# Performance work log

Measured on AMD Instinct MI355X. Metric: run time of the kernel, lower is better.

## Reference

```python
import jax, jax.numpy as jnp
import numpy as np

B, T, IN_DIM = 32, 512, 16
F_DIM, N_AGG, N_HEADS = 128, 32, 4


def _ln(x, g, b, eps=1e-5):
    m = jnp.mean(x, axis=-1, keepdims=True)
    v = jnp.var(x, axis=-1, keepdims=True)
    return (x - m) * jax.lax.rsqrt(v + eps) * g + b


def _masked_sab(X, mask, wq, bq, wk, bk, wv, bv, wo, bo, g0, be0, g1, be1):
    # Set-Transformer style SAB = MAB(X, X) with key-side masking.
    Bn, Tn, _ = X.shape
    Dh = F_DIM // N_HEADS
    Q = X @ wq + bq
    K = X @ wk + bk
    V = X @ wv + bv
    Qh = Q.reshape(Bn, Tn, N_HEADS, Dh)
    Kh = K.reshape(Bn, Tn, N_HEADS, Dh)
    Vh = V.reshape(Bn, Tn, N_HEADS, Dh)
    scores = jnp.einsum('bqhd,bkhd->bhqk', Qh, Kh) / np.float32(np.sqrt(Dh))
    scores = jnp.where(mask[:, None, None, :] > 0, scores, jnp.float32(-1e9))
    A = jax.nn.softmax(scores, axis=-1)
    O = Q + jnp.einsum('bhqk,bkhd->bqhd', A, Vh).reshape(Bn, Tn, F_DIM)
    O = _ln(O, g0, be0)
    O = O + jax.nn.relu(O @ wo + bo)
    return _ln(O, g1, be1)


def setup_inputs():
    key = jax.random.key(0)
    ks = list(jax.random.split(key, 16))

    def g(k, shape):
        return jax.random.uniform(k, shape, jnp.float32, -1.0, 1.0) / np.float32(np.sqrt(shape[0]))

    inp = {
        'X': jax.random.normal(ks[0], (B, T, IN_DIM), dtype=jnp.float32),
        'mask': jax.random.bernoulli(ks[1], 0.8, (B, T)).astype(jnp.float32),
    }
    i = 2
    for suf, din in (('0', IN_DIM), ('1', F_DIM)):
        kk = jax.random.split(ks[i], 4); i += 1
        inp['wq' + suf] = g(kk[0], (din, F_DIM)); inp['bq' + suf] = jnp.zeros((F_DIM,), jnp.float32)
        inp['wk' + suf] = g(kk[1], (din, F_DIM)); inp['bk' + suf] = jnp.zeros((F_DIM,), jnp.float32)
        inp['wv' + suf] = g(kk[2], (din, F_DIM)); inp['bv' + suf] = jnp.zeros((F_DIM,), jnp.float32)
        inp['wo' + suf] = g(kk[3], (F_DIM, F_DIM)); inp['bo' + suf] = jnp.zeros((F_DIM,), jnp.float32)
        inp['g0' + suf] = jnp.ones((F_DIM,), jnp.float32); inp['be0' + suf] = jnp.zeros((F_DIM,), jnp.float32)
        inp['g1' + suf] = jnp.ones((F_DIM,), jnp.float32); inp['be1' + suf] = jnp.zeros((F_DIM,), jnp.float32)
    inp['wti'] = g(ks[i], (F_DIM, F_DIM)); i += 1
    inp['bti'] = jnp.zeros((F_DIM,), jnp.float32)
    inp['was'] = g(ks[i], (F_DIM, N_AGG)); i += 1
    inp['bas'] = jnp.zeros((N_AGG,), jnp.float32)
    d_cat = 2 * F_DIM * N_AGG + IN_DIM + F_DIM
    inp['wto'] = g(ks[i], (d_cat, F_DIM)); i += 1
    inp['bto'] = jnp.zeros((F_DIM,), jnp.float32)
    inp['gto'] = jnp.ones((F_DIM,), jnp.float32)
    inp['btoln'] = jnp.zeros((F_DIM,), jnp.float32)
    return inp


def reference(X, mask, wq0, bq0, wk0, bk0, wv0, bv0, wo0, bo0, g00, be00, g10, be10,
              wq1, bq1, wk1, bk1, wv1, bv1, wo1, bo1, g01, be01, g11, be11,
              wti, bti, was, bas, wto, bto, gto, btoln):
    m = mask[..., None]                                  # [B,T,1]
    Xp = _masked_sab(X, mask, wq0, bq0, wk0, bk0, wv0, bv0, wo0, bo0, g00, be00, g10, be10) * m
    Xp = _masked_sab(Xp, mask, wq1, bq1, wk1, bk1, wv1, bv1, wo1, bo1, g01, be01, g11, be11) * m
    Xp = (Xp @ wti + bti) * m
    # masked softmax over tracks (dim 1); max is taken over ALL tracks as in original
    s = Xp @ was + bas                                   # [B,T,A]
    num = jnp.exp(s - jnp.max(s, axis=1, keepdims=True)) * m
    att = num / (jnp.sum(num, axis=1, keepdims=True) + 1e-16)
    edges = jnp.einsum('btf,bta->baft', Xp, att)         # [B,A,F,T] -- dominant buffer
    min_elem = jnp.min(edges, axis=-1) - 1.0             # [B,A,F]
    mk = mask[:, None, None, :]                          # [B,1,1,T]
    max_pooled = jnp.max(edges * mk + (1.0 - mk) * min_elem[..., None], axis=-1)
    n_tracks = jnp.sum(mask, axis=-1)[:, None, None]
    n_tracks = jnp.where(n_tracks == 0, jnp.float32(1.0), n_tracks)
    mean_pooled = jnp.sum(edges * mk, axis=-1) / n_tracks
    agg = jnp.concatenate([max_pooled, mean_pooled], axis=-1).reshape(X.shape[0], -1)  # [B, 2*F*A]
    agg_rep = jnp.broadcast_to(agg[:, None, :], (X.shape[0], X.shape[1], agg.shape[-1]))
    Hcat = jnp.concatenate([X, Xp, agg_rep], axis=-1)    # [B,T, 2*F*A + in + F]
    out = jax.nn.relu(_ln(Hcat @ wto + bto, gto, btoln)) * m
    return out, agg
```

## Files before the change

### kernel.cpp

```cpp
#include <hip/hip_runtime.h>
#include <hip/hip_bf16.h>

#define BB 32
#define TT 512
#define IND 16
#define FD 128
#define NAGG 32

typedef unsigned short ushortt;
typedef unsigned int uintt;
typedef __attribute__((ext_vector_type(8))) short bf16x8;
typedef __attribute__((ext_vector_type(4))) short s16x4;
typedef __attribute__((ext_vector_type(4))) float f32x4;

__device__ __forceinline__ short f2b(float x) {
  union { __hip_bfloat16 h; short s; } u;
  u.h = __float2bfloat16(x);
  return u.s;
}

#define MFMA_16x16x32(A, B, C) __builtin_amdgcn_mfma_f32_16x16x32_bf16(A, B, C, 0, 0, 0)

#define GEMM128(WT, c00, c01, c10, c11)                                        \
  {                                                                            \
    _Pragma("unroll") for (int ks = 0; ks < 4; ks++) {                         \
      bf16x8 a0 = *(const bf16x8*)&Xb[l15][ks * 32 + g * 8];                   \
      bf16x8 a1 = *(const bf16x8*)&Xb[16 + l15][ks * 32 + g * 8];              \
      bf16x8 b0 = *(const bf16x8*)((WT) + (size_t)c0 * 128 + ks * 32 + g * 8); \
      bf16x8 b1 = *(const bf16x8*)((WT) + (size_t)c1 * 128 + ks * 32 + g * 8); \
      c00 = MFMA_16x16x32(a0, b0, c00);                                        \
      c01 = MFMA_16x16x32(a0, b1, c01);                                        \
      c10 = MFMA_16x16x32(a1, b0, c10);                                        \
      c11 = MFMA_16x16x32(a1, b1, c11);                                        \
    }                                                                          \
  }

__global__ void prep_w_k(const float* __restrict__ wo0, const float* __restrict__ wq1,
                         const float* __restrict__ wk1, const float* __restrict__ wv1,
                         const float* __restrict__ wo1, const float* __restrict__ wti,
                         const float* __restrict__ wto, const float* __restrict__ was,
                         ushortt* __restrict__ Wt) {
  int m = blockIdx.x >> 2;
  int slab = blockIdx.x & 3;
  int tid = threadIdx.x;
  if (m == 7) {
    __shared__ float t[32][33];
    int iloc = tid >> 3, c4 = (tid & 7) * 4;
    *(float4*)&t[iloc][c4] = *(const float4*)(was + (size_t)(slab * 32 + iloc) * 32 + c4);
    __syncthreads();
    int a = tid & 31, ch = tid >> 5;
    short p[4];
#pragma unroll
    for (int k = 0; k < 4; k++) p[k] = f2b(t[ch * 4 + k][a]);
    *(s16x4*)(Wt + (size_t)7 * 16384 + (size_t)a * 128 + slab * 32 + ch * 4) = *(s16x4*)p;
  } else {
    const float* src = m == 0 ? wo0 : m == 1 ? wq1 : m == 2 ? wk1
                     : m == 3 ? wv1 : m == 4 ? wo1 : m == 5 ? wti : wto + IND * FD;
    __shared__ float t[32][132];
    int r = tid >> 3, c16 = (tid & 7) * 16;
    const float4* s4 = (const float4*)(src + (size_t)(slab * 32 + r) * 128 + c16);
#pragma unroll
    for (int jj = 0; jj < 4; jj++) *(float4*)&t[r][c16 + jj * 4] = s4[jj];
    __syncthreads();
    int f = tid >> 1, ih = (tid & 1) * 16;
    short p[16];
#pragma unroll
    for (int k = 0; k < 16; k++) p[k] = f2b(t[ih + k][f]);
    ushortt* dst = Wt + (size_t)m * 16384 + (size_t)f * 128 + slab * 32 + ih;
    *(bf16x8*)dst = *(bf16x8*)&p[0];
    *(bf16x8*)(dst + 8) = *(bf16x8*)&p[8];
  }
}

__global__ void proj16_k(const float* __restrict__ X,
                         const float* __restrict__ wq, const float* __restrict__ bq,
                         const float* __restrict__ wk, const float* __restrict__ bk,
                         const float* __restrict__ wv, const float* __restrict__ bv,
                         float* __restrict__ Q, ushortt* __restrict__ Kb,
                         ushortt* __restrict__ Vt) {
  int base = blockIdx.x * 8;
  int b = base >> 9;
  int tloc = base & 511;
  int f = threadIdx.x;
  __shared__ float xs[8][IND];
  {
    int rr = f >> 4, ii = f & 15;
    xs[rr][ii] = X[(size_t)(base + rr) * IND + ii];
  }
  __syncthreads();
  float qa[8], ka[8], va[8];
  float bqf = bq[f], bkf = bk[f], bvf = bv[f];
#pragma unroll
  for (int rr = 0; rr < 8; rr++) { qa[rr] = bqf; ka[rr] = bkf; va[rr] = bvf; }
#pragma unroll
  for (int i = 0; i < IND; i++) {
    float wqv = wq[i * FD + f], wkv = wk[i * FD + f], wvv = wv[i * FD + f];
#pragma unroll
    for (int rr = 0; rr < 8; rr++) {
      float x = xs[rr][i];
      qa[rr] += x * wqv; ka[rr] += x * wkv; va[rr] += x * wvv;
    }
  }
  short vp[8];
#pragma unroll
  for (int rr = 0; rr < 8; rr++) {
    size_t o = (size_t)(base + rr) * FD + f;
    Q[o] = qa[rr];
    Kb[o] = (ushortt)f2b(ka[rr]);
    vp[rr] = f2b(va[rr]);
  }
  *(bf16x8*)&Vt[((size_t)(b * FD) + f) * 512 + tloc] = *(bf16x8*)vp;
}

__global__ __launch_bounds__(256, 2) void attn_k(const float* __restrict__ Q,
                                                 const ushortt* __restrict__ Kb,
                                                 const ushortt* __restrict__ Vt,
                                                 const float* __restrict__ mask,
                                                 float* __restrict__ Ores) {
  int b = blockIdx.x >> 4;
  int qt = blockIdx.x & 15;
  int tid = threadIdx.x;
  int w = tid >> 6;
  int lane = tid & 63;
  int l15 = lane & 15, g = lane >> 4;

  __shared__ __align__(16) short q_s[32 * 136];
  __shared__ __align__(16) short k_s[2][32 * 136];
  __shared__ __align__(16) short vt_s[2][128 * 40];
  __shared__ __align__(16) short p_s[4][32 * 40];
  __shared__ __align__(16) float msk_s[512];
  __shared__ __align__(16) float xch[4][32];

  const float scale = 0.17677669529663688f;

  msk_s[tid] = mask[b * TT + tid];
  msk_s[256 + tid] = mask[b * TT + 256 + tid];

  int sr = tid >> 3, sc8 = tid & 7;
  size_t qbase = ((size_t)(b * TT + qt * 32 + sr)) * FD + sc8 * 16;
  {
    const float4* src = (const float4*)(Q + qbase);
#pragma unroll
    for (int jj = 0; jj < 4; jj++) {
      float4 v4 = src[jj];
      *(s16x4*)&q_s[sr * 136 + sc8 * 16 + jj * 4] =
          (s16x4){f2b(v4.x * scale), f2b(v4.y * scale), f2b(v4.z * scale),
                  f2b(v4.w * scale)};
    }
  }

  bf16x8 kr[2], vr[2];
  const ushortt* KbB = Kb + (size_t)b * TT * FD;
  const ushortt* VtB = Vt + (size_t)b * FD * 512;

#define LOAD_TILE(kt)                                                              \
  {                                                                                \
    const ushortt* kbp = KbB + (size_t)(kt) * 32 * FD;                             \
    _Pragma("unroll") for (int is = 0; is < 2; is++) {                             \
      int idx = tid + is * 256;                                                    \
      kr[is] = *(const bf16x8*)(kbp + (idx >> 4) * FD + (idx & 15) * 8);           \
      vr[is] = *(const bf16x8*)(VtB + (size_t)(idx >> 2) * 512 + (kt) * 32 +       \
                                (idx & 3) * 8);                                    \
    }                                                                              \
  }
#define WRITE_TILE(buf)                                                            \
  {                                                                                \
    _Pragma("unroll") for (int is = 0; is < 2; is++) {                             \
      int idx = tid + is * 256;                                                    \
      *(bf16x8*)&k_s[buf][(idx >> 4) * 136 + (idx & 15) * 8] = kr[is];             \
      *(bf16x8*)&vt_s[buf][(idx >> 2) * 40 + (idx & 3) * 8] = vr[is];              \
    }                                                                              \
  }

  LOAD_TILE(0);
  WRITE_TILE(0);

  f32x4 o00 = {0.f, 0.f, 0.f, 0.f}, o01 = o00, o10 = o00, o11 = o00;
  float m0 = -1e30f, m1 = -1e30f, l0 = 0.f, l1 = 0.f;

  bf16x8 aq0, aq1;
  int cur = 0;

  for (int kt = 0; kt < 16; kt++) {
    __syncthreads();
    if (kt == 0) {
      aq0 = *(const bf16x8*)&q_s[l15 * 136 + w * 32 + g * 8];
      aq1 = *(const bf16x8*)&q_s[(16 + l15) * 136 + w * 32 + g * 8];
    }
    if (kt < 15) LOAD_TILE(kt + 1);

    bf16x8 bk0 = *(const bf16x8*)&k_s[cur][l15 * 136 + w * 32 + g * 8];
    bf16x8 bk1 = *(const bf16x8*)&k_s[cur][(16 + l15) * 136 + w * 32 + g * 8];
    f32x4 zero = {0.f, 0.f, 0.f, 0.f};
    f32x4 st00 = MFMA_16x16x32(bk0, aq0, zero);
    f32x4 st01 = MFMA_16x16x32(bk0, aq1, zero);
    f32x4 st10 = MFMA_16x16x32(bk1, aq0, zero);
    f32x4 st11 = MFMA_16x16x32(bk1, aq1, zero);

    float4 mk0 = *(const float4*)&msk_s[kt * 32 + 4 * g];
    float4 mk1 = *(const float4*)&msk_s[kt * 32 + 16 + 4 * g];
    float x0[8], x1[8];
#pragma unroll
    for (int r = 0; r < 4; r++) {
      x0[r] = mk0[r] > 0.f ? st00[r] : -1e9f;
      x0[4 + r] = mk1[r] > 0.f ? st10[r] : -1e9f;
      x1[r] = mk0[r] > 0.f ? st01[r] : -1e9f;
      x1[4 + r] = mk1[r] > 0.f ? st11[r] : -1e9f;
    }
    float lm0 = x0[0], lm1 = x1[0];
#pragma unroll
    for (int i = 1; i < 8; i++) { lm0 = fmaxf(lm0, x0[i]); lm1 = fmaxf(lm1, x1[i]); }
    lm0 = fmaxf(lm0, __shfl_xor(lm0, 16));
    lm0 = fmaxf(lm0, __shfl_xor(lm0, 32));
    lm1 = fmaxf(lm1, __shfl_xor(lm1, 16));
    lm1 = fmaxf(lm1, __shfl_xor(lm1, 32));
    bool need = (lm0 > m0 + 8.f) || (lm1 > m1 + 8.f);
    if (__any(need)) {
      float mn0 = fmaxf(m0, lm0), mn1 = fmaxf(m1, lm1);
      float scv0 = __expf(m0 - mn0), scv1 = __expf(m1 - mn1);
      m0 = mn0; m1 = mn1;
      l0 *= scv0; l1 *= scv1;
      if (lane < 16) { xch[w][l15] = scv0; xch[w][16 + l15] = scv1; }
      float4 sa = *(const float4*)&xch[w][4 * g];
      float4 sb = *(const float4*)&xch[w][16 + 4 * g];
#pragma unroll
      for (int r = 0; r < 4; r++) {
        o00[r] *= sa[r]; o01[r] *= sa[r];
        o10[r] *= sb[r]; o11[r] *= sb[r];
      }
    }
    float p0[8], p1[8];
    float rs0 = 0.f, rs1 = 0.f;
#pragma unroll
    for (int i = 0; i < 8; i++) {
      p0[i] = __expf(x0[i] - m0); rs0 += p0[i];
      p1[i] = __expf(x1[i] - m1); rs1 += p1[i];
    }
    rs0 += __shfl_xor(rs0, 16); rs0 += __shfl_xor(rs0, 32);
    rs1 += __shfl_xor(rs1, 16); rs1 += __shfl_xor(rs1, 32);
    l0 += rs0; l1 += rs1;
    {
      uintt a0 = ((uintt)(ushortt)f2b(p0[1]) << 16) | (ushortt)f2b(p0[0]);
      uintt a1 = ((uintt)(ushortt)f2b(p0[3]) << 16) | (ushortt)f2b(p0[2]);
      uintt a2 = ((uintt)(ushortt)f2b(p0[5]) << 16) | (ushortt)f2b(p0[4]);
      uintt a3 = ((uintt)(ushortt)f2b(p0[7]) << 16) | (ushortt)f2b(p0[6]);
      uintt b0 = ((uintt)(ushortt)f2b(p1[1]) << 16) | (ushortt)f2b(p1[0]);
      uintt b1 = ((uintt)(ushortt)f2b(p1[3]) << 16) | (ushortt)f2b(p1[2]);
      uintt b2 = ((uintt)(ushortt)f2b(p1[5]) << 16) | (ushortt)f2b(p1[4]);
      uintt b3 = ((uintt)(ushortt)f2b(p1[7]) << 16) | (ushortt)f2b(p1[6]);
      *(uint2*)&p_s[w][l15 * 40 + 4 * g] = make_uint2(a0, a1);
      *(uint2*)&p_s[w][l15 * 40 + 16 + 4 * g] = make_uint2(a2, a3);
      *(uint2*)&p_s[w][(16 + l15) * 40 + 4 * g] = make_uint2(b0, b1);
      *(uint2*)&p_s[w][(16 + l15) * 40 + 16 + 4 * g] = make_uint2(b2, b3);
    }
    bf16x8 ap0 = *(const bf16x8*)&p_s[w][l15 * 40 + g * 8];
    bf16x8 ap1 = *(const bf16x8*)&p_s[w][(16 + l15) * 40 + g * 8];
    bf16x8 bv0 = *(const bf16x8*)&vt_s[cur][(w * 32 + l15) * 40 + g * 8];
    bf16x8 bv1 = *(const bf16x8*)&vt_s[cur][(w * 32 + 16 + l15) * 40 + g * 8];
    o00 = MFMA_16x16x32(ap0, bv0, o00);
    o01 = MFMA_16x16x32(ap0, bv1, o01);
    o10 = MFMA_16x16x32(ap1, bv0, o10);
    o11 = MFMA_16x16x32(ap1, bv1, o11);

    if (kt < 15) WRITE_TILE(cur ^ 1);
    cur ^= 1;
  }
  if (lane < 16) { xch[w][l15] = l0; xch[w][16 + l15] = l1; }
  float4 la = *(const float4*)&xch[w][4 * g];
  float4 lb = *(const float4*)&xch[w][16 + 4 * g];
  size_t rowbase = (size_t)(b * TT + qt * 32);
#pragma unroll
  for (int r = 0; r < 4; r++) {
    int q0r = 4 * g + r;
    size_t base0 = (rowbase + q0r) * FD + w * 32 + l15;
    Ores[base0] = Q[base0] + o00[r] / la[r];
    Ores[base0 + 16] = Q[base0 + 16] + o01[r] / la[r];
    int q1r = 16 + 4 * g + r;
    size_t base1 = (rowbase + q1r) * FD + w * 32 + l15;
    Ores[base1] = Q[base1] + o10[r] / lb[r];
    Ores[base1 + 16] = Q[base1 + 16] + o11[r] / lb[r];
  }
#undef LOAD_TILE
#undef WRITE_TILE
}

__device__ __forceinline__ void ln32(float (*A)[132], short (*Xb)[136], int lane, int w,
                                     const float* __restrict__ gg,
                                     const float* __restrict__ bb,
                                     const float* mk, bool applyMask) {
  float ga = gg[lane], gb = gg[lane + 64], ba = bb[lane], b2 = bb[lane + 64];
  for (int j = 0; j < 8; j++) {
    int rr = w * 8 + j;
    float a = A[rr][lane], c = A[rr][lane + 64];
    float s = a + c, ss = a * a + c * c;
#pragma unroll
    for (int o = 32; o > 0; o >>= 1) { s += __shfl_xor(s, o); ss += __shfl_xor(ss, o); }
    float mean = s * (1.f / 128.f);
    float var = ss * (1.f / 128.f) - mean * mean;
    float rs = rsqrtf(var + 1e-5f);
    float m = applyMask ? mk[rr] : 1.f;
    float y0 = ((a - mean) * rs * ga + ba) * m;
    float y1 = ((c - mean) * rs * gb + b2) * m;
    A[rr][lane] = y0; A[rr][lane + 64] = y1;
    Xb[rr][lane] = f2b(y0); Xb[rr][lane + 64] = f2b(y1);
  }
}

__global__ __launch_bounds__(256) void post_proj_k(
    const float* __restrict__ Ores, const float* __restrict__ mask,
    const ushortt* __restrict__ wot, const float* __restrict__ bo,
    const float* __restrict__ g0, const float* __restrict__ be0,
    const float* __restrict__ g1, const float* __restrict__ be1,
    const ushortt* __restrict__ wqt, const float* __restrict__ bq,
    const ushortt* __restrict__ wkt, const float* __restrict__ bk,
    const ushortt* __restrict__ wvt, const float* __restrict__ bv,
    float* __restrict__ Q, ushortt* __restrict__ Kb, ushortt* __restrict__ Vt) {
  int base = blockIdx.x * 32;
  int b = base >> 9;
  int tloc = base & 511;
  int tid = threadIdx.x;
  int w = tid >> 6, lane = tid & 63;
  int l15 = lane & 15, g = lane >> 4;

  __shared__ float A32[32][132];
  __shared__ __align__(16) short Xb[32][136];
  __shared__ float mk[32];

  {
    int r = tid >> 3, c = (tid & 7) * 16;
    const float4* src = (const float4*)(Ores + (size_t)(base + r) * FD + c);
#pragma unroll
    for (int jj = 0; jj < 4; jj++) *(float4*)&A32[r][c + jj * 4] = src[jj];
  }
  if (tid < 32) mk[tid] = mask[base + tid];
  __syncthreads();
  ln32(A32, Xb, lane, w, g0, be0, mk, false);
  __syncthreads();

  int c0 = w * 32 + l15, c1 = c0 + 16;
  f32x4 f00 = {0.f, 0.f, 0.f, 0.f}, f01 = f00, f10 = f00, f11 = f00;
  GEMM128(wot, f00, f01, f10, f11);
  float bo0 = bo[c0], bo1 = bo[c1];
#pragma unroll
  for (int r = 0; r < 4; r++) {
    int r0 = g * 4 + r, r1 = 16 + r0;
    A32[r0][c0] += fmaxf(f00[r] + bo0, 0.f);
    A32[r0][c1] += fmaxf(f01[r] + bo1, 0.f);
    A32[r1][c0] += fmaxf(f10[r] + bo0, 0.f);
    A32[r1][c1] += fmaxf(f11[r] + bo1, 0.f);
  }
  __syncthreads();
  ln32(A32, Xb, lane, w, g1, be1, mk, true);
  __syncthreads();

  {
    f32x4 q00 = {0.f, 0.f, 0.f, 0.f}, q01 = q00, q10 = q00, q11 = q00;
    GEMM128(wqt, q00, q01, q10, q11);
    float bq0 = bq[c0], bq1 = bq[c1];
#pragma unroll
    for (int r = 0; r < 4; r++) {
      int r0 = g * 4 + r, r1 = 16 + r0;
      Q[(size_t)(base + r0) * FD + c0] = q00[r] + bq0;
      Q[(size_t)(base + r0) * FD + c1] = q01[r] + bq1;
      Q[(size_t)(base + r1) * FD + c0] = q10[r] + bq0;
      Q[(size_t)(base + r1) * FD + c1] = q11[r] + bq1;
    }
  }
  {
    f32x4 k00 = {0.f, 0.f, 0.f, 0.f}, k01 = k00, k10 = k00, k11 = k00;
    GEMM128(wkt, k00, k01, k10, k11);
    float bk0 = bk[c0], bk1 = bk[c1];
#pragma unroll
    for (int r = 0; r < 4; r++) {
      int r0 = g * 4 + r, r1 = 16 + r0;
      Kb[(size_t)(base + r0) * FD + c0] = (ushortt)f2b(k00[r] + bk0);
      Kb[(size_t)(base + r0) * FD + c1] = (ushortt)f2b(k01[r] + bk1);
      Kb[(size_t)(base + r1) * FD + c0] = (ushortt)f2b(k10[r] + bk0);
      Kb[(size_t)(base + r1) * FD + c1] = (ushortt)f2b(k11[r] + bk1);
    }
  }
  {
    f32x4 v00 = {0.f, 0.f, 0.f, 0.f}, v01 = v00, v10 = v00, v11 = v00;
    GEMM128(wvt, v00, v01, v10, v11);
    float bv0 = bv[c0], bv1 = bv[c1];
    short p[4];
#pragma unroll
    for (int k = 0; k < 4; k++) p[k] = f2b(v00[k] + bv0);
    *(s16x4*)&Vt[((size_t)b * FD + c0) * 512 + tloc + g * 4] = *(s16x4*)p;
#pragma unroll
    for (int k = 0; k < 4; k++) p[k] = f2b(v01[k] + bv1);
    *(s16x4*)&Vt[((size_t)b * FD + c1) * 512 + tloc + g * 4] = *(s16x4*)p;
#pragma unroll
    for (int k = 0; k < 4; k++) p[k] = f2b(v10[k] + bv0);
    *(s16x4*)&Vt[((size_t)b * FD + c0) * 512 + tloc + 16 + g * 4] = *(s16x4*)p;
#pragma unroll
    for (int k = 0; k < 4; k++) p[k] = f2b(v11[k] + bv1);
    *(s16x4*)&Vt[((size_t)b * FD + c1) * 512 + tloc + 16 + g * 4] = *(s16x4*)p;
  }
}

__global__ __launch_bounds__(256) void post_ti_k(
    const float* __restrict__ Ores, const float* __restrict__ mask,
    const ushortt* __restrict__ wot, const float* __restrict__ bo,
    const float* __restrict__ g0, const float* __restrict__ be0,
    const float* __restrict__ g1, const float* __restrict__ be1,
    const ushortt* __restrict__ wtit, const float* __restrict__ bti,
    const ushortt* __restrict__ wast, const float* __restrict__ bas,
    float* __restrict__ Xp2, float* __restrict__ S) {
  int base = blockIdx.x * 32;
  int tid = threadIdx.x;
  int w = tid >> 6, lane = tid & 63;
  int l15 = lane & 15, g = lane >> 4;

  __shared__ float A32[32][132];
  __shared__ __align__(16) short Xb[32][136];
  __shared__ float mk[32];

  {
    int r = tid >> 3, c = (tid & 7) * 16;
    const float4* src = (const float4*)(Ores + (size_t)(base + r) * FD + c);
#pragma unroll
    for (int jj = 0; jj < 4; jj++) *(float4*)&A32[r][c + jj * 4] = src[jj];
  }
  if (tid < 32) mk[tid] = mask[base + tid];
  __syncthreads();
  ln32(A32, Xb, lane, w, g0, be0, mk, false);
  __syncthreads();

  int c0 = w * 32 + l15, c1 = c0 + 16;
  f32x4 f00 = {0.f, 0.f, 0.f, 0.f}, f01 = f00, f10 = f00, f11 = f00;
  GEMM128(wot, f00, f01, f10, f11);
  float bo0 = bo[c0], bo1 = bo[c1];
#pragma unroll
  for (int r = 0; r < 4; r++) {
    int r0 = g * 4 + r, r1 = 16 + r0;
    A32[r0][c0] += fmaxf(f00[r] + bo0, 0.f);
    A32[r0][c1] += fmaxf(f01[r] + bo1, 0.f);
    A32[r1][c0] += fmaxf(f10[r] + bo0, 0.f);
    A32[r1][c1] += fmaxf(f11[r] + bo1, 0.f);
  }
  __syncthreads();
  ln32(A32, Xb, lane, w, g1, be1, mk, true);
  __syncthreads();

  f32x4 t00 = {0.f, 0.f, 0.f, 0.f}, t01 = t00, t10 = t00, t11 = t00;
  GEMM128(wtit, t00, t01, t10, t11);
  float bti0 = bti[c0], bti1 = bti[c1];
  short pk[16];
#pragma unroll
  for (int r = 0; r < 4; r++) {
    int r0 = g * 4 + r, r1 = 16 + r0;
    float v00 = (t00[r] + bti0) * mk[r0];
    float v01 = (t01[r] + bti1) * mk[r0];
    float v10 = (t10[r] + bti0) * mk[r1];
    float v11 = (t11[r] + bti1) * mk[r1];
    Xp2[(size_t)(base + r0) * FD + c0] = v00;
    Xp2[(size_t)(base + r0) * FD + c1] = v01;
    Xp2[(size_t)(base + r1) * FD + c0] = v10;
    Xp2[(size_t)(base + r1) * FD + c1] = v11;
    pk[r * 4 + 0] = f2b(v00);
    pk[r * 4 + 1] = f2b(v01);
    pk[r * 4 + 2] = f2b(v10);
    pk[r * 4 + 3] = f2b(v11);
  }
  __syncthreads();
#pragma unroll
  for (int r = 0; r < 4; r++) {
    int r0 = g * 4 + r, r1 = 16 + r0;
    Xb[r0][c0] = pk[r * 4 + 0];
    Xb[r0][c1] = pk[r * 4 + 1];
    Xb[r1][c0] = pk[r * 4 + 2];
    Xb[r1][c1] = pk[r * 4 + 3];
  }
  __syncthreads();
  if (w < 2) {
    int a0 = w * 16 + l15;
    f32x4 s0 = {0.f, 0.f, 0.f, 0.f}, s1 = s0;
#pragma unroll
    for (int ks = 0; ks < 4; ks++) {
      bf16x8 aa0 = *(const bf16x8*)&Xb[l15][ks * 32 + g * 8];
      bf16x8 aa1 = *(const bf16x8*)&Xb[16 + l15][ks * 32 + g * 8];
      bf16x8 bb0 = *(const bf16x8*)(wast + (size_t)a0 * 128 + ks * 32 + g * 8);
      s0 = MFMA_16x16x32(aa0, bb0, s0);
      s1 = MFMA_16x16x32(aa1, bb0, s1);
    }
    float bas0 = bas[a0];
#pragma unroll
    for (int r = 0; r < 4; r++) {
      int r0 = g * 4 + r;
      S[(size_t)(base + r0) * NAGG + a0] = s0[r] + bas0;
      S[(size_t)(base + 16 + r0) * NAGG + a0] = s1[r] + bas0;
    }
  }
}

__global__ void soft_t(const float* __restrict__ S, const float* __restrict__ mask,
                       float* __restrict__ att) {
  int b = blockIdx.x >> 5, a = blockIdx.x & 31;
  int tid = threadIdx.x;
  __shared__ float red[2];
  float sv[4], mv[4];
#pragma unroll
  for (int j = 0; j < 4; j++) {
    int t = tid + j * 128;
    sv[j] = S[(size_t)(b * TT + t) * NAGG + a];
    mv[j] = mask[b * TT + t];
  }
  float mx = fmaxf(fmaxf(sv[0], sv[1]), fmaxf(sv[2], sv[3]));
#pragma unroll
  for (int o = 32; o > 0; o >>= 1) mx = fmaxf(mx, __shfl_xor(mx, o));
  if ((tid & 63) == 0) red[tid >> 6] = mx;
  __syncthreads();
  mx = fmaxf(red[0], red[1]);
  __syncthreads();
  float e[4];
  float sm = 0.f;
#pragma unroll
  for (int j = 0; j < 4; j++) {
    e[j] = __expf(sv[j] - mx) * mv[j];
    sm += e[j];
  }
#pragma unroll
  for (int o = 32; o > 0; o >>= 1) sm += __shfl_xor(sm, o);
  if ((tid & 63) == 0) red[tid >> 6] = sm;
  __syncthreads();
  float inv = 1.f / (red[0] + red[1] + 1e-16f);
  float* dst = att + ((size_t)(b * NAGG + a)) * TT;
#pragma unroll
  for (int j = 0; j < 4; j++) dst[tid + j * 128] = e[j] * inv;
}

__global__ void pool_part_k(const float* __restrict__ Xp2, const float* __restrict__ att,
                            const float* __restrict__ mask,
                            float* __restrict__ pmax, float* __restrict__ pmin,
                            float* __restrict__ psum) {
  int bid = blockIdx.x;
  int b = bid >> 7;
  int a = (bid >> 2) & 31;
  int tc = bid & 3;
  int f = threadIdx.x;
  __shared__ float att_s[128];
  __shared__ float ms[128];
  att_s[f] = att[((size_t)(b * NAGG + a)) * TT + tc * 128 + f];
  ms[f] = mask[b * TT + tc * 128 + f];
  __syncthreads();
  const float* xp = Xp2 + ((size_t)(b * TT + tc * 128)) * FD + f;
  float mn = 1e30f, mx = -1e30f, sm = 0.f;
#pragma unroll 4
  for (int t = 0; t < 128; t++) {
    float e = xp[(size_t)t * FD] * att_s[t];
    mn = fminf(mn, e);
    bool keep = ms[t] > 0.f;
    mx = keep ? fmaxf(mx, e) : mx;
    sm = keep ? sm + e : sm;
  }
  size_t idx = (size_t)bid * 128 + f;
  pmax[idx] = mx;
  pmin[idx] = mn;
  psum[idx] = sm;
}

__global__ void combine_k(const float* __restrict__ pmax, const float* __restrict__ pmin,
                          const float* __restrict__ psum, const float* __restrict__ mask,
                          float* __restrict__ aggF, float* __restrict__ agg_out) {
  int b = blockIdx.x >> 5, a = blockIdx.x & 31;
  int f = threadIdx.x;
  __shared__ float red[2];
  float ntp = 0.f;
#pragma unroll
  for (int j = 0; j < 4; j++) ntp += (mask[b * TT + f + j * 128] > 0.f) ? 1.f : 0.f;
#pragma unroll
  for (int o = 32; o > 0; o >>= 1) ntp += __shfl_xor(ntp, o);
  if ((f & 63) == 0) red[f >> 6] = ntp;
  __syncthreads();
  float nt = red[0] + red[1];
  float mx = -1e30f, mn = 1e30f, sm = 0.f;
#pragma unroll
  for (int tc = 0; tc < 4; tc++) {
    size_t idx = ((size_t)(b * 128 + a * 4 + tc)) * 128 + f;
    mx = fmaxf(mx, pmax[idx]);
    mn = fminf(mn, pmin[idx]);
    sm += psum[idx];
  }
  bool anyUn = nt < 511.5f;
  float mp = anyUn ? fmaxf(mx, mn - 1.f) : mx;
  float mean = sm / (nt == 0.f ? 1.f : nt);
  size_t bs = (size_t)b * 8192 + (size_t)a * 256;
  aggF[bs + f] = mp;
  aggF[bs + 128 + f] = mean;
  agg_out[bs + f] = mp;
  agg_out[bs + 128 + f] = mean;
}

__global__ void aggmm_k(const float* __restrict__ aggF, const float* __restrict__ wto,
                        float* __restrict__ part) {
  int b = blockIdx.x >> 5, cc = blockIdx.x & 31;
  int f = threadIdx.x;
  __shared__ float ag[256];
  ag[f] = aggF[(size_t)b * 8192 + cc * 256 + f];
  ag[128 + f] = aggF[(size_t)b * 8192 + cc * 256 + 128 + f];
  __syncthreads();
  const float* w = wto + ((size_t)(IND + FD) + cc * 256) * FD;
  float a0 = 0.f, a1 = 0.f, a2 = 0.f, a3 = 0.f;
#pragma unroll 4
  for (int j = 0; j < 256; j += 4) {
    a0 += ag[j] * w[(size_t)j * FD + f];
    a1 += ag[j + 1] * w[(size_t)(j + 1) * FD + f];
    a2 += ag[j + 2] * w[(size_t)(j + 2) * FD + f];
    a3 += ag[j + 3] * w[(size_t)(j + 3) * FD + f];
  }
  part[(size_t)(b * 32 + cc) * FD + f] = (a0 + a1) + (a2 + a3);
}

__global__ __launch_bounds__(256) void final_k(
    const float* __restrict__ X, const float* __restrict__ Xp2,
    const float* __restrict__ part, const ushortt* __restrict__ wtot,
    const float* __restrict__ wto, const float* __restrict__ bto,
    const float* __restrict__ gto, const float* __restrict__ btoln,
    const float* __restrict__ mask, float* __restrict__ out) {
  int base = blockIdx.x * 32;
  int b = base >> 9;
  int tid = threadIdx.x;
  int w = tid >> 6, lane = tid & 63;
  int l15 = lane & 15, g = lane >> 4;
  __shared__ float A32[32][132];
  __shared__ __align__(16) short Xb[32][136];
  __shared__ float xss[32][17];
  __shared__ float psum_s[128];
  __shared__ float mk[32];
  {
    int r = tid >> 3, c = (tid & 7) * 16;
    const float4* src = (const float4*)(Xp2 + (size_t)(base + r) * FD + c);
#pragma unroll
    for (int jj = 0; jj < 4; jj++) {
      float4 v = src[jj];
      *(s16x4*)&Xb[r][c + jj * 4] = (s16x4){f2b(v.x), f2b(v.y), f2b(v.z), f2b(v.w)};
    }
  }
  {
    int r = tid >> 3, ii = (tid & 7) * 2;
    xss[r][ii] = X[(size_t)(base + r) * IND + ii];
    xss[r][ii + 1] = X[(size_t)(base + r) * IND + ii + 1];
  }
  if (tid < 32) mk[tid] = mask[base + tid];
  if (tid < 128) {
    float ps = 0.f;
#pragma unroll 8
    for (int cc = 0; cc < 32; cc++) ps += part[(size_t)(b * 32 + cc) * FD + tid];
    psum_s[tid] = ps;
  }
  __syncthreads();
  int c0 = w * 32 + l15, c1 = c0 + 16;
  f32x4 q00 = {0.f, 0.f, 0.f, 0.f}, q01 = q00, q10 = q00, q11 = q00;
  GEMM128(wtot, q00, q01, q10, q11);
  float wx0[16], wx1[16];
#pragma unroll
  for (int i = 0; i < 16; i++) { wx0[i] = wto[i * FD + c0]; wx1[i] = wto[i * FD + c1]; }
  float add0 = bto[c0] + psum_s[c0], add1 = bto[c1] + psum_s[c1];
#pragma unroll
  for (int r = 0; r < 4; r++) {
    int r0 = g * 4 + r, r1 = 16 + r0;
    float x00 = q00[r] + add0, x01 = q01[r] + add1;
    float x10 = q10[r] + add0, x11 = q11[r] + add1;
#pragma unroll
    for (int i = 0; i < 16; i++) {
      x00 += xss[r0][i] * wx0[i];
      x01 += xss[r0][i] * wx1[i];
      x10 += xss[r1][i] * wx0[i];
      x11 += xss[r1][i] * wx1[i];
    }
    A32[r0][c0] = x00; A32[r0][c1] = x01;
    A32[r1][c0] = x10; A32[r1][c1] = x11;
  }
  __syncthreads();
  float ga = gto[lane], gb = gto[lane + 64], ba = btoln[lane], bb2 = btoln[lane + 64];
  for (int j = 0; j < 8; j++) {
    int rr = w * 8 + j;
    float a = A32[rr][lane], c = A32[rr][lane + 64];
    float s = a + c, ss = a * a + c * c;
#pragma unroll
    for (int o = 32; o > 0; o >>= 1) { s += __shfl_xor(s, o); ss += __shfl_xor(ss, o); }
    float mean = s * (1.f / 128.f);
    float var = ss * (1.f / 128.f) - mean * mean;
    float rs = rsqrtf(var + 1e-5f);
    float m = mk[rr];
    out[(size_t)(base + rr) * FD + lane] = fmaxf((a - mean) * rs * ga + ba, 0.f) * m;
    out[(size_t)(base + rr) * FD + lane + 64] = fmaxf((c - mean) * rs * gb + bb2, 0.f) * m;
  }
}

extern "C" void kernel_launch(void* const* d_in, const int* in_sizes, int n_in,
                              void* d_out, int out_size, void* d_ws, size_t ws_size,
                              hipStream_t stream) {
  const float* X    = (const float*)d_in[0];
  const float* mask = (const float*)d_in[1];
  const float* wq0 = (const float*)d_in[2];  const float* bq0 = (const float*)d_in[3];
  const float* wk0 = (const float*)d_in[4];  const float* bk0 = (const float*)d_in[5];
  const float* wv0 = (const float*)d_in[6];  const float* bv0 = (const float*)d_in[7];
  const float* wo0 = (const float*)d_in[8];  const float* bo0 = (const float*)d_in[9];
  const float* g00 = (const float*)d_in[10]; const float* be00 = (const float*)d_in[11];
  const float* g10 = (const float*)d_in[12]; const float* be10 = (const float*)d_in[13];
  const float* wq1 = (const float*)d_in[14]; const float* bq1 = (const float*)d_in[15];
  const float* wk1 = (const float*)d_in[16]; const float* bk1 = (const float*)d_in[17];
  const float* wv1 = (const float*)d_in[18]; const float* bv1 = (const float*)d_in[19];
  const float* wo1 = (const float*)d_in[20]; const float* bo1 = (const float*)d_in[21];
  const float* g01 = (const float*)d_in[22]; const float* be01 = (const float*)d_in[23];
  const float* g11 = (const float*)d_in[24]; const float* be11 = (const float*)d_in[25];
  const float* wti = (const float*)d_in[26]; const float* bti = (const float*)d_in[27];
  const float* was = (const float*)d_in[28]; const float* bas = (const float*)d_in[29];
  const float* wto = (const float*)d_in[30]; const float* bto = (const float*)d_in[31];
  const float* gto = (const float*)d_in[32]; const float* btoln = (const float*)d_in[33];

  const size_t BIG = (size_t)BB * TT * FD;
  float* ws = (float*)d_ws;
  float* Qf = ws;
  ushortt* Kb = (ushortt*)(ws + BIG);
  ushortt* Vt = (ushortt*)(ws + BIG + BIG / 2);
  float* Ores = Qf;
  float* Xp2 = ws + BIG;
  float* S    = ws + 2 * BIG;
  float* att  = ws + 2 * BIG + 524288;
  float* aggF = ws + 2 * BIG + 1048576;
  float* part = ws + 2 * BIG + 1310720;
  ushortt* Wt = (ushortt*)(ws + 2 * BIG + 1441792);
  float* pmax = ws;
  float* pmin = ws + 524288;
  float* psum = ws + 1048576;

  ushortt* wo0t = Wt;
  ushortt* wq1t = Wt + 16384;
  ushortt* wk1t = Wt + 2 * 16384;
  ushortt* wv1t = Wt + 3 * 16384;
  ushortt* wo1t = Wt + 4 * 16384;
  ushortt* wtit = Wt + 5 * 16384;
  ushortt* wtot = Wt + 6 * 16384;
  ushortt* wast = Wt + 7 * 16384;

  float* out_main = (float*)d_out;
  float* out_agg  = (float*)d_out + BIG;

  int nrb = BB * TT / 8;
  int nrb32 = BB * TT / 32;
  prep_w_k<<<32, 256, 0, stream>>>(wo0, wq1, wk1, wv1, wo1, wti, wto, was, Wt);
  proj16_k<<<nrb, 128, 0, stream>>>(X, wq0, bq0, wk0, bk0, wv0, bv0, Qf, Kb, Vt);
  attn_k<<<BB * 16, 256, 0, stream>>>(Qf, Kb, Vt, mask, Ores);
  post_proj_k<<<nrb32, 256, 0, stream>>>(Ores, mask, wo0t, bo0, g00, be00, g10, be10,
                                         wq1t, bq1, wk1t, bk1, wv1t, bv1, Qf, Kb, Vt);
  attn_k<<<BB * 16, 256, 0, stream>>>(Qf, Kb, Vt, mask, Ores);
  post_ti_k<<<nrb32, 256, 0, stream>>>(Ores, mask, wo1t, bo1, g01, be01, g11, be11,
                                       wtit, bti, wast, bas, Xp2, S);
  soft_t<<<BB * NAGG, 128, 0, stream>>>(S, mask, att);
  pool_part_k<<<BB * NAGG * 4, 128, 0, stream>>>(Xp2, att, mask, pmax, pmin, psum);
  combine_k<<<BB * NAGG, 128, 0, stream>>>(pmax, pmin, psum, mask, aggF, out_agg);
  aggmm_k<<<BB * 32, 128, 0, stream>>>(aggF, wto, part);
  final_k<<<nrb32, 256, 0, stream>>>(X, Xp2, part, wtot, wto, bto, gto, btoln, mask, out_main);
}
```

Before: 145.0 us.

## Tile pooling kernel over agg heads with shared-memory staging of Xp

Rewrites the pooling partial kernel so each block stages a 128x64 tile of Xp and 16 attention rows in shared memory. Each thread then accumulates max, min and sum for 4 aggregation heads at once, instead of reading Xp from global memory once per head. The partial-result layout is reordered, and combine_k's indexing is updated to match. In exchange the grid shrinks to 512 blocks and each block uses more LDS and registers.

Result: no change. 144.9 us (median of 2 runs) (-0.1%).

```diff
diff --git a/kernel.cpp b/kernel.cpp
--- a/kernel.cpp
+++ b/kernel.cpp
@@ -530,34 +530,61 @@
   for (int j = 0; j < 4; j++) dst[tid + j * 128] = e[j] * inv;
 }
 
-__global__ void pool_part_k(const float* __restrict__ Xp2, const float* __restrict__ att,
-                            const float* __restrict__ mask,
-                            float* __restrict__ pmax, float* __restrict__ pmin,
-                            float* __restrict__ psum) {
+__global__ __launch_bounds__(256) void pool_k2(const float* __restrict__ Xp2,
+                                               const float* __restrict__ att,
+                                               const float* __restrict__ mask,
+                                               float* __restrict__ pmax,
+                                               float* __restrict__ pmin,
+                                               float* __restrict__ psum) {
   int bid = blockIdx.x;
-  int b = bid >> 7;
-  int a = (bid >> 2) & 31;
-  int tc = bid & 3;
-  int f = threadIdx.x;
-  __shared__ float att_s[128];
+  int b = bid >> 4;
+  int tc = (bid >> 2) & 3;
+  int fg = (bid >> 1) & 1;
+  int ag = bid & 1;
+  int tid = threadIdx.x;
+  __shared__ float xp_s[128][68];
+  __shared__ float att_s[16][128];
   __shared__ float ms[128];
-  att_s[f] = att[((size_t)(b * NAGG + a)) * TT + tc * 128 + f];
-  ms[f] = mask[b * TT + tc * 128 + f];
-  __syncthreads();
-  const float* xp = Xp2 + ((size_t)(b * TT + tc * 128)) * FD + f;
-  float mn = 1e30f, mx = -1e30f, sm = 0.f;
+  {
+    int r = tid >> 1, half = tid & 1;
+    const float4* src =
+        (const float4*)(Xp2 + ((size_t)(b * TT + tc * 128 + r)) * FD + fg * 64 + half * 32);
+#pragma unroll
+    for (int j = 0; j < 8; j++) *(float4*)&xp_s[r][half * 32 + j * 4] = src[j];
+  }
+  {
+    int a = tid >> 4, t8 = (tid & 15) * 8;
+    const float4* src =
+        (const float4*)(att + ((size_t)(b * NAGG + ag * 16 + a)) * TT + tc * 128 + t8);
+    *(float4*)&att_s[a][t8] = src[0];
+    *(float4*)&att_s[a][t8 + 4] = src[1];
+  }
+  if (tid < 128) ms[tid] = mask[b * TT + tc * 128 + tid];
+  __syncthreads();
+  int fl = tid & 63, h = tid >> 6;
+  float mn[4], mx[4], sm[4];
+#pragma unroll
+  for (int a = 0; a < 4; a++) { mn[a] = 1e30f; mx[a] = -1e30f; sm[a] = 0.f; }
 #pragma unroll 4
   for (int t = 0; t < 128; t++) {
-    float e = xp[(size_t)t * FD] * att_s[t];
-    mn = fminf(mn, e);
+    float e0 = xp_s[t][fl];
     bool keep = ms[t] > 0.f;
-    mx = keep ? fmaxf(mx, e) : mx;
-    sm = keep ? sm + e : sm;
-  }
-  size_t idx = (size_t)bid * 128 + f;
-  pmax[idx] = mx;
-  pmin[idx] = mn;
-  psum[idx] = sm;
+#pragma unroll
+    for (int a = 0; a < 4; a++) {
+      float e = e0 * att_s[h * 4 + a][t];
+      mn[a] = fminf(mn[a], e);
+      mx[a] = keep ? fmaxf(mx[a], e) : mx[a];
+      sm[a] = keep ? sm[a] + e : sm[a];
+    }
+  }
+#pragma unroll
+  for (int a = 0; a < 4; a++) {
+    int aa = ag * 16 + h * 4 + a;
+    size_t idx = ((size_t)((b * 4 + tc) * 32 + aa)) * 128 + fg * 64 + fl;
+    pmax[idx] = mx[a];
+    pmin[idx] = mn[a];
+    psum[idx] = sm[a];
+  }
 }
 
 __global__ void combine_k(const float* __restrict__ pmax, const float* __restrict__ pmin,
@@ -577,7 +604,7 @@
   float mx = -1e30f, mn = 1e30f, sm = 0.f;
 #pragma unroll
   for (int tc = 0; tc < 4; tc++) {
-    size_t idx = ((size_t)(b * 128 + a * 4 + tc)) * 128 + f;
+    size_t idx = ((size_t)((b * 4 + tc) * 32 + a)) * 128 + f;
     mx = fmaxf(mx, pmax[idx]);
     mn = fminf(mn, pmin[idx]);
     sm += psum[idx];
@@ -750,7 +777,7 @@
   post_ti_k<<<nrb32, 256, 0, stream>>>(Ores, mask, wo1t, bo1, g01, be01, g11, be11,
                                        wtit, bti, wast, bas, Xp2, S);
   soft_t<<<BB * NAGG, 128, 0, stream>>>(S, mask, att);
-  pool_part_k<<<BB * NAGG * 4, 128, 0, stream>>>(Xp2, att, mask, pmax, pmin, psum);
+  pool_k2<<<BB * 16, 256, 0, stream>>>(Xp2, att, mask, pmax, pmin, psum);
   combine_k<<<BB * NAGG, 128, 0, stream>>>(pmax, pmin, psum, mask, aggF, out_agg);
   aggmm_k<<<BB * 32, 128, 0, stream>>>(aggF, wto, part);
   final_k<<<nrb32, 256, 0, stream>>>(X, Xp2, part, wtot, wto, bto, gto, btoln, mask, out_main);
```
